# Kernel optimization log

Measured on AMD Instinct MI355X. Metric: run time of the kernel, lower is better.

## Reference

```python
import jax, jax.numpy as jnp
from jax import lax
import numpy as np

B, S, H, L = 64, 512, 768, 9

def setup_inputs() -> dict:
    key = jax.random.key(0)
    ks = jax.random.split(key, 8)
    return {
        'hidden': jax.random.normal(ks[0], (B, S, H), dtype=jnp.float32),
        'W': jax.random.normal(ks[1], (H, L), dtype=jnp.float32) * 0.02,
        'b': jax.random.normal(ks[2], (L,), dtype=jnp.float32) * 0.02,
        'start_transitions': jax.random.normal(ks[3], (L,), dtype=jnp.float32) * 0.1,
        'transitions': jax.random.normal(ks[4], (L, L), dtype=jnp.float32) * 0.1,
        'end_transitions': jax.random.normal(ks[5], (L,), dtype=jnp.float32) * 0.1,
        'labels': jax.random.randint(ks[6], (B, S), 0, L, dtype=jnp.int64),
        'lengths': jax.random.randint(ks[7], (B,), 0, S, dtype=jnp.int32),
    }

def _crf_nll(emissions, labels, mask, start_transitions, transitions, end_transitions):
    # emissions [B,S,L], labels [B,S] int, mask [B,S] bool (mask[:,0] all True)
    Bv = emissions.shape[0]
    bidx = jnp.arange(Bv)
    fmask = mask.astype(emissions.dtype)
    # --- numerator: score of the gold path ---
    t0 = labels[:, 0]
    score0 = start_transitions[t0] + emissions[bidx, 0, t0]  # [B]
    def num_step(score, xs):
        em_t, tag_prev, tag_t, m_t = xs  # [B,L],[B],[B],[B]
        inc = transitions[tag_prev, tag_t] + em_t[bidx, tag_t]
        return score + inc * m_t, None
    num_xs = (jnp.swapaxes(emissions[:, 1:], 0, 1),  # [S-1,B,L]
              labels[:, :-1].T, labels[:, 1:].T, fmask[:, 1:].T)
    numerator, _ = lax.scan(num_step, score0, num_xs)
    seq_ends = jnp.sum(mask, axis=1) - 1  # [B]
    last_tags = labels[bidx, seq_ends]
    numerator = numerator + end_transitions[last_tags]
    # --- denominator: forward algorithm (logsumexp DP) ---
    alpha0 = start_transitions[None, :] + emissions[:, 0]  # [B,L]
    def den_step(alpha, xs):
        em_t, m_t = xs  # [B,L], [B] bool
        nxt = jax.scipy.special.logsumexp(
            alpha[:, :, None] + transitions[None, :, :] + em_t[:, None, :], axis=1)
        return jnp.where(m_t[:, None], nxt, alpha), None
    den_xs = (jnp.swapaxes(emissions[:, 1:], 0, 1), mask[:, 1:].T)
    alpha, _ = lax.scan(den_step, alpha0, den_xs)
    denominator = jax.scipy.special.logsumexp(alpha + end_transitions[None, :], axis=1)
    # torchcrf forward returns sum of log-likelihoods (reduction='sum'); model negates
    return -jnp.sum(numerator - denominator)

def reference(hidden, W, b, start_transitions, transitions, end_transitions, labels, lengths):
    # dropout is identity at inference; BERT output is modeled by `hidden`
    emissions = jnp.einsum('bsh,hl->bsl', hidden, W) + b  # [B,S,L]
    lens = jnp.maximum(lengths, 1)  # torchcrf requires mask[:,0] on
    mask = jnp.arange(emissions.shape[1])[None, :] < lens[:, None]  # [B,S]
    return _crf_nll(emissions, labels, mask, start_transitions, transitions, end_transitions)
```

## Files before the change

### kernel.cpp

```cpp
#include <hip/hip_runtime.h>

#define B_ 64
#define S_ 512
#define H_ 768
#define L_ 9
#define EMP 16
#define CH 16
#define NCHUNK 32
#define CPAD 88

typedef __attribute__((ext_vector_type(8))) short bf16x8;
typedef __attribute__((ext_vector_type(4))) float f32x4;
typedef bf16x8 __attribute__((may_alias)) bf16x8_a;
typedef uint2  __attribute__((may_alias)) uint2_a;

__device__ __forceinline__ int eoff(int t) { return t * 12 + (t >> 4) * 4; }

__device__ __forceinline__ unsigned pack_bf16(float lo, float hi) {
    unsigned a = __float_as_uint(lo) + 0x8000u;
    unsigned b = __float_as_uint(hi) + 0x8000u;
    return __builtin_amdgcn_perm(b, a, 0x07060302);
}

__global__ __launch_bounds__(512) void emis_kernel(
    const float* __restrict__ hidden, const float* __restrict__ W,
    const float* __restrict__ bias, const int* __restrict__ lengths,
    float* __restrict__ em, float* __restrict__ out)
{
    __shared__ unsigned Wl[96 * 16 * 4];
    __shared__ float bias16[16];
    __shared__ unsigned hbuf[8][2][16 * 36];

    const int T = threadIdx.x;
    if (blockIdx.x == 0 && T == 0) out[0] = 0.0f;

    const int g = blockIdx.x;

    const int wv = T >> 6, lane = T & 63;
    const int q = lane >> 4, col = lane & 15;

    const int b   = (g + 9 * wv) & 63;
    const int pos = 4 * wv + ((g >> 6) ^ (wv & 3));
    const int s0  = pos * 16;
    int len = lengths[b]; if (len < 1) len = 1;
    const bool tile_live = (s0 < len);
    const int row_abs = (b << 9) + s0;

    const int srow = lane >> 2, sm = lane & 3;
    const float* hrow = hidden + (size_t)(row_abs + srow) * H_ + sm * 4;

    float4 L[2][4];
    if (tile_live) {
        #pragma unroll
        for (int m = 0; m < 4; ++m) L[0][m] = *(const float4*)(hrow + m * 16);
        #pragma unroll
        for (int m = 0; m < 4; ++m) L[1][m] = *(const float4*)(hrow + 64 + m * 16);
    }

    if (T < 16) bias16[T] = (T < 9) ? bias[T] : 0.0f;
    #pragma unroll
    for (int r3 = 0; r3 < 3; ++r3) {
        const int sidx = T + 512 * r3;
        const int k8 = sidx >> 4, c = sidx & 15;
        unsigned w0 = 0, w1 = 0, w2 = 0, w3 = 0;
        if (c < 9) {
            const float* wp = W + (size_t)(k8 * 8) * 9 + c;
            w0 = pack_bf16(wp[0],  wp[9]);
            w1 = pack_bf16(wp[18], wp[27]);
            w2 = pack_bf16(wp[36], wp[45]);
            w3 = pack_bf16(wp[54], wp[63]);
        }
        uint4 v = { w0, w1, w2, w3 };
        *(uint4*)&Wl[sidx * 4] = v;
    }
    __syncthreads();

    if (!tile_live) return;

    unsigned* buf0 = &hbuf[wv][0][0];
    unsigned* buf1 = &hbuf[wv][1][0];
    const int woff = srow * 36 + sm * 2;
    const int rdoff = col * 36 + q * 4;

    #pragma unroll
    for (int m = 0; m < 4; ++m) {
        uint2 u = { pack_bf16(L[0][m].x, L[0][m].y),
                    pack_bf16(L[0][m].z, L[0][m].w) };
        *(uint2_a*)(buf0 + woff + m * 8) = u;
    }

    const float4 bias4 = *(const float4*)(bias16 + q * 4);
    f32x4 acc = { 0.0f, 0.0f, 0.0f, 0.0f };

    #pragma unroll
    for (int p = 0; p < 12; ++p) {
        unsigned* cbuf = (p & 1) ? buf1 : buf0;
        unsigned* nbuf = (p & 1) ? buf0 : buf1;

        if (p + 2 < 12) {
            #pragma unroll
            for (int m = 0; m < 4; ++m)
                L[p & 1][m] = *(const float4*)(hrow + (p + 2) * 64 + m * 16);
        }

        #pragma unroll
        for (int s = 0; s < 2; ++s) {
            const bf16x8 bu = *(const bf16x8_a*)(cbuf + rdoff + s * 16);
            const uint4 a4 =
                *(const uint4*)&Wl[(((p * 2 + s) * 4 + q) * 16 + col) * 4];
            union { unsigned u[4]; bf16x8 v; } au;
            au.u[0] = a4.x; au.u[1] = a4.y; au.u[2] = a4.z; au.u[3] = a4.w;
            acc = __builtin_amdgcn_mfma_f32_16x16x32_bf16(au.v, bu, acc, 0, 0, 0);
        }

        if (p + 1 < 12) {
            #pragma unroll
            for (int m = 0; m < 4; ++m) {
                uint2 u = { pack_bf16(L[(p + 1) & 1][m].x, L[(p + 1) & 1][m].y),
                            pack_bf16(L[(p + 1) & 1][m].z, L[(p + 1) & 1][m].w) };
                *(uint2_a*)(nbuf + woff + m * 8) = u;
            }
        }
    }

    const int srow_out = s0 + col;
    if (srow_out < len) {
        float4 o = { acc[0] + bias4.x, acc[1] + bias4.y,
                     acc[2] + bias4.z, acc[3] + bias4.w };
        *(float4*)(em + (size_t)((b << 9) + srow_out) * EMP + q * 4) = o;
    }
}

__global__ __launch_bounds__(384, 1) void crf_kernel(
    const float* __restrict__ em, const int* __restrict__ labels,
    const int* __restrict__ lengths, const float* __restrict__ start_t,
    const float* __restrict__ trans, const float* __restrict__ end_t,
    float* __restrict__ out)
{
    __shared__ float eem[6288];
    __shared__ float Pl[112];
    __shared__ float Cs[NCHUNK * CPAD];
    __shared__ float Cs2[16 * CPAD];
    __shared__ float rmx_s[16 * 12];
    __shared__ float lgA[32], lgB[16];
    const int T = threadIdx.x;
    const int b = blockIdx.x;
    int len = lengths[b]; if (len < 1) len = 1;

    if (T < 81) {
        const int k = T / 9, j = T - 9 * k;
        Pl[k * 12 + j] = __expf(trans[T]);
    }
    #pragma unroll
    for (int r = 0; r < 2; ++r) {
        const int t = T + 384 * r;
        if (t < len) {
            const int o = eoff(t);
            const float4* p = (const float4*)(em + (size_t)((b << 9) + t) * EMP);
            float4 v0 = p[0], v1 = p[1], v2 = p[2];
            float4 w0 = { __expf(v0.x), __expf(v0.y), __expf(v0.z), __expf(v0.w) };
            float4 w1 = { __expf(v1.x), __expf(v1.y), __expf(v1.z), __expf(v1.w) };
            *(float4*)(eem + o) = w0;
            *(float4*)(eem + o + 4) = w1;
            eem[o + 8] = __expf(v2.x);
        }
    }
    if (T < 32) lgA[T] = 0.0f;
    __syncthreads();

    if (T < 288) {
        const int c = T / 9;
        const int i = T - 9 * c;
        float A[9];
        #pragma unroll
        for (int j = 0; j < 9; ++j) A[j] = (i == j) ? 1.0f : 0.0f;
        const int t0 = CH * c + 1;

        #pragma unroll 1
        for (int s = 0; s < CH; ++s) {
            const int t = t0 + s;
            const int o = eoff(t);
            float4 e0 = *(const float4*)(eem + o);
            float4 e1 = *(const float4*)(eem + o + 4);
            const float e8 = eem[o + 8];
            const float e[9] = { e0.x, e0.y, e0.z, e0.w,
                                 e1.x, e1.y, e1.z, e1.w, e8 };

            float an[9];
            #pragma unroll
            for (int j = 0; j < 9; ++j) an[j] = 0.0f;
            #pragma unroll
            for (int k = 0; k < 9; ++k) {
                float4 p0 = *(const float4*)(Pl + k * 12);
                float4 p1 = *(const float4*)(Pl + k * 12 + 4);
                const float p8 = Pl[k * 12 + 8];
                const float pr[9] = { p0.x, p0.y, p0.z, p0.w,
                                      p1.x, p1.y, p1.z, p1.w, p8 };
                const float ak = A[k];
                #pragma unroll
                for (int j = 0; j < 9; ++j)
                    an[j] = fmaf(ak, pr[j], an[j]);
            }
            const bool live = (t < len);
            #pragma unroll
            for (int j = 0; j < 9; ++j)
                A[j] = live ? an[j] * e[j] : A[j];
            if (s == 7) {
                #pragma unroll
                for (int j = 0; j < 9; ++j) A[j] *= 0x1p-40f;
            }
        }
        #pragma unroll
        for (int j = 0; j < 9; ++j) Cs[c * CPAD + i * 9 + j] = A[j];
    } else if (T >= 320) {
        const int lane = T - 320;
        const int* lab = labels + (size_t)b * S_;
        float part = 0.0f;
        for (int t = 1 + lane; t < len; t += 64) {
            const int tp = lab[t - 1], tc = lab[t];
            part += trans[tp * 9 + tc] + em[(size_t)((b << 9) + t) * EMP + tc];
        }
        #pragma unroll
        for (int off = 32; off >= 1; off >>= 1) part += __shfl_xor(part, off, 64);
        if (lane == 0) {
            const int l0 = lab[0], le = lab[len - 1];
            const float num = start_t[l0] + em[(size_t)(b << 9) * EMP + l0]
                            + part + end_t[le];
            atomicAdd(out, -num);
        }
    }
    __syncthreads();

    float* src = Cs;  float* dst = Cs2;
    float* ls  = lgA; float* ld  = lgB;
    int nn = 16;
    #pragma unroll 1
    for (int lvl = 0; lvl < 5; ++lvl) {
        const int n = T / 9, i = T - 9 * n;
        float row[9];
        if (T < nn * 9) {
            const float* Am = src + (2 * n) * CPAD;
            const float* Bm = src + (2 * n + 1) * CPAD;
            float a[9];
            #pragma unroll
            for (int k = 0; k < 9; ++k) a[k] = Am[i * 9 + k];
            #pragma unroll
            for (int j = 0; j < 9; ++j) row[j] = 0.0f;
            #pragma unroll
            for (int k = 0; k < 9; ++k) {
                const float ak = a[k];
                #pragma unroll
                for (int j = 0; j < 9; ++j)
                    row[j] = fmaf(ak, Bm[k * 9 + j], row[j]);
            }
            float rmx = row[0];
            #pragma unroll
            for (int j = 1; j < 9; ++j) rmx = fmaxf(rmx, row[j]);
            rmx_s[n * 12 + i] = rmx;
        }
        __syncthreads();
        if (T < nn * 9) {
            float mx = rmx_s[n * 12];
            #pragma unroll
            for (int k = 1; k < 9; ++k) mx = fmaxf(mx, rmx_s[n * 12 + k]);
            const float inv = 1.0f / mx;
            #pragma unroll
            for (int j = 0; j < 9; ++j) dst[n * CPAD + i * 9 + j] = row[j] * inv;
            if (i == 0) ld[n] = ls[2 * n] + ls[2 * n + 1] + __logf(mx);
        }
        __syncthreads();
        float* t1 = src; src = dst; dst = t1;
        float* t2 = ls;  ls = ld;  ld = t2;
        nn >>= 1;
    }

    if (T == 0) {
        const float4* e0 = (const float4*)(em + (size_t)(b << 9) * EMP);
        float4 v0 = e0[0], v1 = e0[1], v2 = e0[2];
        float al[9] = { v0.x + start_t[0], v0.y + start_t[1], v0.z + start_t[2],
                        v0.w + start_t[3], v1.x + start_t[4], v1.y + start_t[5],
                        v1.z + start_t[6], v1.w + start_t[7], v2.x + start_t[8] };
        float m0 = al[0];
        #pragma unroll
        for (int j = 1; j < 9; ++j) m0 = fmaxf(m0, al[j]);
        float alpha[9];
        #pragma unroll
        for (int j = 0; j < 9; ++j) alpha[j] = __expf(al[j] - m0);

        float ev = 0.0f;
        #pragma unroll
        for (int j = 0; j < 9; ++j) {
            float s = 0.0f;
            #pragma unroll
            for (int i = 0; i < 9; ++i)
                s = fmaf(alpha[i], src[i * 9 + j], s);
            ev = fmaf(s, __expf(end_t[j]), ev);
        }
        const float den = m0 + ls[0] + __logf(ev)
                        + 1280.0f * 0.6931471805599453f;
        atomicAdd(out, den);
    }
}

extern "C" void kernel_launch(void* const* d_in, const int* in_sizes, int n_in,
                              void* d_out, int out_size, void* d_ws, size_t ws_size,
                              hipStream_t stream)
{
    (void)in_sizes; (void)n_in; (void)out_size; (void)ws_size;
    const float* hidden  = (const float*)d_in[0];
    const float* W       = (const float*)d_in[1];
    const float* bias    = (const float*)d_in[2];
    const float* start_t = (const float*)d_in[3];
    const float* trans   = (const float*)d_in[4];
    const float* end_t   = (const float*)d_in[5];
    const int*   labels  = (const int*)d_in[6];
    const int*   lengths = (const int*)d_in[7];

    float* em  = (float*)d_ws;
    float* out = (float*)d_out;

    emis_kernel<<<256, 512, 0, stream>>>(hidden, W, bias, lengths, em, out);
    crf_kernel<<<B_, 384, 0, stream>>>(em, labels, lengths,
                                       start_t, trans, end_t, out);
}
```

Measured before the change: 27.90 us.

## Split emission GEMM along K and add atomic work-stealing queue for load balance

The emission projection now splits each 16-row tile into two K-halves written to separate buffers (em0 with bias, em1 without), and the CRF kernel sums the halves when loading. Waves fetch tiles dynamically from per-group atomic counters instead of a fixed assignment, so waves whose tiles are past the sequence length pick up more work. This targets load imbalance from variable-length sequences but adds a memset launch, atomics, and twice the emission traffic read in the CRF kernel.

```diff
diff --git a/kernel.cpp b/kernel.cpp
--- a/kernel.cpp
+++ b/kernel.cpp
@@ -25,7 +25,8 @@
 __global__ __launch_bounds__(512) void emis_kernel(
     const float* __restrict__ hidden, const float* __restrict__ W,
     const float* __restrict__ bias, const int* __restrict__ lengths,
-    float* __restrict__ em, float* __restrict__ out)
+    float* __restrict__ em0, float* __restrict__ em1,
+    int* __restrict__ ctr, float* __restrict__ out)
 {
     __shared__ unsigned Wl[96 * 16 * 4];
     __shared__ float bias16[16];
@@ -35,27 +36,12 @@
     if (blockIdx.x == 0 && T == 0) out[0] = 0.0f;
 
     const int g = blockIdx.x;
+    const int grp = g & 7;
+    const int sblk = g >> 3;
 
     const int wv = T >> 6, lane = T & 63;
     const int q = lane >> 4, col = lane & 15;
-
-    const int b   = (g + 9 * wv) & 63;
-    const int pos = 4 * wv + ((g >> 6) ^ (wv & 3));
-    const int s0  = pos * 16;
-    int len = lengths[b]; if (len < 1) len = 1;
-    const bool tile_live = (s0 < len);
-    const int row_abs = (b << 9) + s0;
-
     const int srow = lane >> 2, sm = lane & 3;
-    const float* hrow = hidden + (size_t)(row_abs + srow) * H_ + sm * 4;
-
-    float4 L[2][4];
-    if (tile_live) {
-        #pragma unroll
-        for (int m = 0; m < 4; ++m) L[0][m] = *(const float4*)(hrow + m * 16);
-        #pragma unroll
-        for (int m = 0; m < 4; ++m) L[1][m] = *(const float4*)(hrow + 64 + m * 16);
-    }
 
     if (T < 16) bias16[T] = (T < 9) ? bias[T] : 0.0f;
     #pragma unroll
@@ -75,67 +61,99 @@
     }
     __syncthreads();
 
-    if (!tile_live) return;
-
     unsigned* buf0 = &hbuf[wv][0][0];
     unsigned* buf1 = &hbuf[wv][1][0];
     const int woff = srow * 36 + sm * 2;
     const int rdoff = col * 36 + q * 4;
-
-    #pragma unroll
-    for (int m = 0; m < 4; ++m) {
-        uint2 u = { pack_bf16(L[0][m].x, L[0][m].y),
-                    pack_bf16(L[0][m].z, L[0][m].w) };
-        *(uint2_a*)(buf0 + woff + m * 8) = u;
-    }
-
     const float4 bias4 = *(const float4*)(bias16 + q * 4);
-    f32x4 acc = { 0.0f, 0.0f, 0.0f, 0.0f };
-
-    #pragma unroll
-    for (int p = 0; p < 12; ++p) {
-        unsigned* cbuf = (p & 1) ? buf1 : buf0;
-        unsigned* nbuf = (p & 1) ? buf0 : buf1;
-
-        if (p + 2 < 12) {
-            #pragma unroll
-            for (int m = 0; m < 4; ++m)
-                L[p & 1][m] = *(const float4*)(hrow + (p + 2) * 64 + m * 16);
-        }
-
-        #pragma unroll
-        for (int s = 0; s < 2; ++s) {
-            const bf16x8 bu = *(const bf16x8_a*)(cbuf + rdoff + s * 16);
-            const uint4 a4 =
-                *(const uint4*)&Wl[(((p * 2 + s) * 4 + q) * 16 + col) * 4];
-            union { unsigned u[4]; bf16x8 v; } au;
-            au.u[0] = a4.x; au.u[1] = a4.y; au.u[2] = a4.z; au.u[3] = a4.w;
-            acc = __builtin_amdgcn_mfma_f32_16x16x32_bf16(au.v, bu, acc, 0, 0, 0);
-        }
-
-        if (p + 1 < 12) {
+    int* myctr = ctr + grp * 16;
+
+    int item = sblk * 8 + wv;
+
+    #pragma unroll 1
+    for (;;) {
+        const int gitem = (grp << 9) + item;
+        const int kh   = gitem & 1;
+        const int tile = gitem >> 1;
+        const int b    = tile >> 5;
+        const int s0   = (tile & 31) << 4;
+        int len = lengths[b]; if (len < 1) len = 1;
+
+        if (s0 < len) {
+            const float* hrow = hidden
+                + (size_t)((b << 9) + s0 + srow) * H_ + kh * 384 + sm * 4;
+
+            float4 L[2][4];
+            #pragma unroll
+            for (int m = 0; m < 4; ++m) L[0][m] = *(const float4*)(hrow + m * 16);
+            #pragma unroll
+            for (int m = 0; m < 4; ++m) L[1][m] = *(const float4*)(hrow + 64 + m * 16);
+
             #pragma unroll
             for (int m = 0; m < 4; ++m) {
-                uint2 u = { pack_bf16(L[(p + 1) & 1][m].x, L[(p + 1) & 1][m].y),
-                            pack_bf16(L[(p + 1) & 1][m].z, L[(p + 1) & 1][m].w) };
-                *(uint2_a*)(nbuf + woff + m * 8) = u;
-            }
-        }
-    }
-
-    const int srow_out = s0 + col;
-    if (srow_out < len) {
-        float4 o = { acc[0] + bias4.x, acc[1] + bias4.y,
-                     acc[2] + bias4.z, acc[3] + bias4.w };
-        *(float4*)(em + (size_t)((b << 9) + srow_out) * EMP + q * 4) = o;
+                uint2 u = { pack_bf16(L[0][m].x, L[0][m].y),
+                            pack_bf16(L[0][m].z, L[0][m].w) };
+                *(uint2_a*)(buf0 + woff + m * 8) = u;
+            }
+
+            f32x4 acc = { 0.0f, 0.0f, 0.0f, 0.0f };
+            #pragma unroll
+            for (int p = 0; p < 6; ++p) {
+                unsigned* cbuf = (p & 1) ? buf1 : buf0;
+                unsigned* nbuf = (p & 1) ? buf0 : buf1;
+
+                if (p + 2 < 6) {
+                    #pragma unroll
+                    for (int m = 0; m < 4; ++m)
+                        L[p & 1][m] = *(const float4*)(hrow + (p + 2) * 64 + m * 16);
+                }
+                #pragma unroll
+                for (int s = 0; s < 2; ++s) {
+                    const bf16x8 bu = *(const bf16x8_a*)(cbuf + rdoff + s * 16);
+                    const int k8 = kh * 48 + (p * 2 + s) * 4 + q;
+                    const uint4 a4 = *(const uint4*)&Wl[(k8 * 16 + col) * 4];
+                    union { unsigned u[4]; bf16x8 v; } au;
+                    au.u[0] = a4.x; au.u[1] = a4.y; au.u[2] = a4.z; au.u[3] = a4.w;
+                    acc = __builtin_amdgcn_mfma_f32_16x16x32_bf16(au.v, bu, acc, 0, 0, 0);
+                }
+                if (p + 1 < 6) {
+                    #pragma unroll
+                    for (int m = 0; m < 4; ++m) {
+                        uint2 u = { pack_bf16(L[(p + 1) & 1][m].x, L[(p + 1) & 1][m].y),
+                                    pack_bf16(L[(p + 1) & 1][m].z, L[(p + 1) & 1][m].w) };
+                        *(uint2_a*)(nbuf + woff + m * 8) = u;
+                    }
+                }
+            }
+
+            const int srow_out = s0 + col;
+            if (srow_out < len) {
+                float4 o;
+                if (kh == 0) {
+                    o.x = acc[0] + bias4.x; o.y = acc[1] + bias4.y;
+                    o.z = acc[2] + bias4.z; o.w = acc[3] + bias4.w;
+                } else {
+                    o.x = acc[0]; o.y = acc[1]; o.z = acc[2]; o.w = acc[3];
+                }
+                float* dst = (kh ? em1 : em0)
+                           + (size_t)((b << 9) + srow_out) * EMP + q * 4;
+                *(float4*)dst = o;
+            }
+        }
+
+        int r;
+        if (lane == 0) r = atomicAdd(myctr, 1);
+        r = __shfl(r, 0, 64);
+        if (r >= 256) break;
+        item = 256 + r;
     }
 }
 
 __global__ __launch_bounds__(384, 1) void crf_kernel(
-    const float* __restrict__ em, const int* __restrict__ labels,
-    const int* __restrict__ lengths, const float* __restrict__ start_t,
-    const float* __restrict__ trans, const float* __restrict__ end_t,
-    float* __restrict__ out)
+    const float* __restrict__ em0, const float* __restrict__ em1,
+    const int* __restrict__ labels, const int* __restrict__ lengths,
+    const float* __restrict__ start_t, const float* __restrict__ trans,
+    const float* __restrict__ end_t, float* __restrict__ out)
 {
     __shared__ float eem[6288];
     __shared__ float Pl[112];
@@ -156,13 +174,18 @@
         const int t = T + 384 * r;
         if (t < len) {
             const int o = eoff(t);
-            const float4* p = (const float4*)(em + (size_t)((b << 9) + t) * EMP);
-            float4 v0 = p[0], v1 = p[1], v2 = p[2];
-            float4 w0 = { __expf(v0.x), __expf(v0.y), __expf(v0.z), __expf(v0.w) };
-            float4 w1 = { __expf(v1.x), __expf(v1.y), __expf(v1.z), __expf(v1.w) };
+            const size_t off = (size_t)((b << 9) + t) * EMP;
+            const float4* p0 = (const float4*)(em0 + off);
+            const float4* p1 = (const float4*)(em1 + off);
+            float4 a0 = p0[0], a1 = p0[1], a2 = p0[2];
+            float4 b0 = p1[0], b1 = p1[1], b2 = p1[2];
+            float4 w0 = { __expf(a0.x + b0.x), __expf(a0.y + b0.y),
+                          __expf(a0.z + b0.z), __expf(a0.w + b0.w) };
+            float4 w1 = { __expf(a1.x + b1.x), __expf(a1.y + b1.y),
+                          __expf(a1.z + b1.z), __expf(a1.w + b1.w) };
             *(float4*)(eem + o) = w0;
             *(float4*)(eem + o + 4) = w1;
-            eem[o + 8] = __expf(v2.x);
+            eem[o + 8] = __expf(a2.x + b2.x);
         }
     }
     if (T < 32) lgA[T] = 0.0f;
@@ -218,13 +241,15 @@
         float part = 0.0f;
         for (int t = 1 + lane; t < len; t += 64) {
             const int tp = lab[t - 1], tc = lab[t];
-            part += trans[tp * 9 + tc] + em[(size_t)((b << 9) + t) * EMP + tc];
+            const size_t idx = (size_t)((b << 9) + t) * EMP + tc;
+            part += trans[tp * 9 + tc] + em0[idx] + em1[idx];
         }
         #pragma unroll
         for (int off = 32; off >= 1; off >>= 1) part += __shfl_xor(part, off, 64);
         if (lane == 0) {
             const int l0 = lab[0], le = lab[len - 1];
-            const float num = start_t[l0] + em[(size_t)(b << 9) * EMP + l0]
+            const size_t i0 = (size_t)(b << 9) * EMP + l0;
+            const float num = start_t[l0] + em0[i0] + em1[i0]
                             + part + end_t[le];
             atomicAdd(out, -num);
         }
@@ -275,11 +300,16 @@
     }
 
     if (T == 0) {
-        const float4* e0 = (const float4*)(em + (size_t)(b << 9) * EMP);
-        float4 v0 = e0[0], v1 = e0[1], v2 = e0[2];
-        float al[9] = { v0.x + start_t[0], v0.y + start_t[1], v0.z + start_t[2],
-                        v0.w + start_t[3], v1.x + start_t[4], v1.y + start_t[5],
-                        v1.z + start_t[6], v1.w + start_t[7], v2.x + start_t[8] };
+        const size_t off0 = (size_t)(b << 9) * EMP;
+        const float4* p0 = (const float4*)(em0 + off0);
+        const float4* p1 = (const float4*)(em1 + off0);
+        float4 a0 = p0[0], a1 = p0[1], a2 = p0[2];
+        float4 b0 = p1[0], b1 = p1[1], b2 = p1[2];
+        float al[9] = { a0.x + b0.x + start_t[0], a0.y + b0.y + start_t[1],
+                        a0.z + b0.z + start_t[2], a0.w + b0.w + start_t[3],
+                        a1.x + b1.x + start_t[4], a1.y + b1.y + start_t[5],
+                        a1.z + b1.z + start_t[6], a1.w + b1.w + start_t[7],
+                        a2.x + b2.x + start_t[8] };
         float m0 = al[0];
         #pragma unroll
         for (int j = 1; j < 9; ++j) m0 = fmaxf(m0, al[j]);
@@ -316,10 +346,14 @@
     const int*   labels  = (const int*)d_in[6];
     const int*   lengths = (const int*)d_in[7];
 
-    float* em  = (float*)d_ws;
+    float* em0 = (float*)d_ws;
+    float* em1 = em0 + (size_t)B_ * S_ * EMP;
+    int*   ctr = (int*)(em1 + (size_t)B_ * S_ * EMP);
     float* out = (float*)d_out;
 
-    emis_kernel<<<256, 512, 0, stream>>>(hidden, W, bias, lengths, em, out);
-    crf_kernel<<<B_, 384, 0, stream>>>(em, labels, lengths,
+    hipMemsetAsync(ctr, 0, 8 * 16 * sizeof(int), stream);
+    emis_kernel<<<256, 512, 0, stream>>>(hidden, W, bias, lengths,
+                                         em0, em1, ctr, out);
+    crf_kernel<<<B_, 384, 0, stream>>>(em0, em1, labels, lengths,
                                        start_t, trans, end_t, out);
 }
```

After: 39.40 us. +41.2%, slower.
